# Kernel tuning notes

Hardware: AMD Instinct MI355X
Metric: run time of the kernel (lower is better)

Reference implementation:

```python
import jax, jax.numpy as jnp
import numpy as np

N_NODES = 20000
N_EDGES = 200000
N_GRAPHS = 128
IN_DIM = 256
HID = 512
HEADS = 8
C = HID // HEADS  # 64
LAT = 256
NEG_SLOPE = 0.2
BN_EPS = 1e-5


def setup_inputs() -> dict:
    key = jax.random.key(0)
    ks = jax.random.split(key, 24)
    n = lambda k, s, sc=0.05: jax.random.normal(k, s, jnp.float32) * sc
    return {
        'x': jax.random.normal(ks[0], (N_NODES, IN_DIM), jnp.float32),
        'edge_index': jax.random.randint(ks[1], (2, N_EDGES), 0, N_NODES, jnp.int32),
        'batch': jnp.sort(jax.random.randint(ks[2], (N_NODES,), 0, N_GRAPHS, jnp.int32)),
        'Wl0': n(ks[3], (IN_DIM, HID)), 'bl0': n(ks[4], (HID,)),
        'Wr0': n(ks[5], (IN_DIM, HID)), 'br0': n(ks[6], (HID,)),
        'att0': n(ks[7], (HEADS, C)), 'bias0': n(ks[8], (HID,)),
        'Wl1': n(ks[9], (HID, HID)), 'bl1': n(ks[10], (HID,)),
        'Wr1': n(ks[11], (HID, HID)), 'br1': n(ks[12], (HID,)),
        'att1': n(ks[13], (HEADS, C)), 'bias1': n(ks[14], (HID,)),
        'bn_gamma': jnp.ones((HID,), jnp.float32),
        'bn_beta': jnp.zeros((HID,), jnp.float32),
        'bn_mean': n(ks[15], (HID,)),
        'bn_var': jax.random.uniform(ks[16], (HID,), jnp.float32, 0.5, 1.5),
        'Wfc': n(ks[17], (HID, LAT)), 'bfc': n(ks[18], (LAT,)),
    }


def gatv2_layer(x, src, dst, Wl, bl, Wr, br, att, bias):
    # x: [N, F]; returns [N, HEADS*C]. GATv2: e = a . LeakyReLU(Wl x_src + Wr x_dst)
    xl = (x @ Wl + bl).reshape(-1, HEADS, C)  # source transform [N,H,C]
    xr = (x @ Wr + br).reshape(-1, HEADS, C)  # target transform [N,H,C]
    feat = jax.nn.leaky_relu(xl[src] + xr[dst], NEG_SLOPE)     # [E,H,C]
    logits = jnp.einsum('ehc,hc->eh', feat, att)               # [E,H]
    # segment softmax over incoming edges of each target node
    m = jax.ops.segment_max(logits, dst, num_segments=N_NODES)  # [N,H]
    p = jnp.exp(logits - m[dst])
    denom = jax.ops.segment_sum(p, dst, num_segments=N_NODES)   # [N,H]
    alpha = p / (denom[dst] + 1e-16)                            # [E,H]
    msg = xl[src] * alpha[:, :, None]                           # [E,H,C]
    out = jax.ops.segment_sum(msg, dst, num_segments=N_NODES)   # [N,H,C]
    return out.reshape(-1, HEADS * C) + bias


def reference(x, edge_index, batch, Wl0, bl0, Wr0, br0, att0, bias0,
              Wl1, bl1, Wr1, br1, att1, bias1,
              bn_gamma, bn_beta, bn_mean, bn_var, Wfc, bfc):
    src, dst = edge_index[0], edge_index[1]
    # layer 0 + ELU (dropout is identity in eval mode)
    h = jax.nn.elu(gatv2_layer(x, src, dst, Wl0, bl0, Wr0, br0, att0, bias0))
    # layer 1 + ELU
    h = jax.nn.elu(gatv2_layer(h, src, dst, Wl1, bl1, Wr1, br1, att1, bias1))
    # global add pool over graphs
    g = jax.ops.segment_sum(h, batch, num_segments=N_GRAPHS)  # [G, HID]
    # BatchNorm1d (eval mode: running stats)
    g = (g - bn_mean) * jax.lax.rsqrt(bn_var + BN_EPS) * bn_gamma + bn_beta
    return g @ Wfc + bfc  # [G, LAT]
```

## Files before the change

kernel.cpp:

```cpp
#include <hip/hip_runtime.h>
#include <hip/hip_bf16.h>
#include <cstdint>

#define NN 20000
#define NE 200000
#define NG 128
#define HID 512
#define XLR_W 1024

typedef __attribute__((ext_vector_type(4))) float f32x4;
typedef __attribute__((ext_vector_type(8))) short s16x8;

__device__ __forceinline__ float bf2f(unsigned short u) {
  union { unsigned int i; float f; } v; v.i = ((unsigned int)u) << 16; return v.f;
}
__device__ __forceinline__ unsigned short f2bf(float f) {
  union { float f; unsigned int i; } v; v.f = f;
  unsigned int i = v.i + 0x7FFFu + ((v.i >> 16) & 1u);
  return (unsigned short)(i >> 16);
}
__device__ __forceinline__ float asf(unsigned int u) {
  union { unsigned int i; float f; } v; v.i = u; return v.f;
}

__global__ void k_cast(const float* __restrict__ in, unsigned short* __restrict__ out, int n4) {
  int i = blockIdx.x * blockDim.x + threadIdx.x;
  if (i < n4) {
    float4 v = ((const float4*)in)[i];
    ushort4 o;
    o.x = f2bf(v.x); o.y = f2bf(v.y); o.z = f2bf(v.z); o.w = f2bf(v.w);
    ((ushort4*)out)[i] = o;
  }
}

__global__ void k_hist(const int* __restrict__ dst, int* __restrict__ deg, int E) {
  int i = blockIdx.x * blockDim.x + threadIdx.x;
  if (i < E) atomicAdd(&deg[dst[i]], 1);
}

__global__ void k_scan(const int* __restrict__ deg, int* __restrict__ offs,
                       int* __restrict__ woff, int n) {
  __shared__ int wsum[16];
  __shared__ int carry;
  int t = threadIdx.x;
  int wid = t >> 6, lane = t & 63;
  if (t == 0) carry = 0;
  __syncthreads();
  for (int base = 0; base < n; base += 1024) {
    int i = base + t;
    int v = (i < n) ? deg[i] : 0;
    int s = v;
#pragma unroll
    for (int off = 1; off < 64; off <<= 1) {
      int x = __shfl_up(s, off, 64);
      if (lane >= off) s += x;
    }
    if (lane == 63) wsum[wid] = s;
    __syncthreads();
    if (wid == 0) {
      int ws = (lane < 16) ? wsum[lane] : 0;
#pragma unroll
      for (int off = 1; off < 16; off <<= 1) {
        int x = __shfl_up(ws, off, 64);
        if (lane >= off) ws += x;
      }
      if (lane < 16) wsum[lane] = ws;
    }
    __syncthreads();
    int c0 = carry;
    int ex = s - v + (wid ? wsum[wid - 1] : 0) + c0;
    if (i < n) { offs[i] = ex; woff[i] = ex; }
    int tot = wsum[15];
    __syncthreads();
    if (t == 0) carry = c0 + tot;
    __syncthreads();
  }
  if (t == 0) offs[n] = carry;
}

__global__ void k_scatter(const int* __restrict__ src, const int* __restrict__ dst,
                          int* __restrict__ woff, int* __restrict__ src_s, int E) {
  int i = blockIdx.x * blockDim.x + threadIdx.x;
  if (i < E) {
    int d = dst[i];
    int pos = atomicAdd(&woff[d], 1);
    src_s[pos] = src[i];
  }
}

__global__ void k_pack(const float* __restrict__ Wl, const float* __restrict__ bl,
                       const float* __restrict__ Wr, const float* __restrict__ br,
                       unsigned short* __restrict__ wt, float* __restrict__ bcat, int kshift) {
  int id = blockIdx.x * blockDim.x + threadIdx.x;
  int K = 1 << kshift;
  int total = XLR_W << kshift;
  if (id < total) {
    int nrow = id >> kshift, k = id & (K - 1);
    float v = (nrow < HID) ? Wl[k * HID + nrow] : Wr[k * HID + (nrow - HID)];
    wt[id] = f2bf(v);
  }
  if (id < XLR_W) bcat[id] = (id < HID) ? bl[id] : br[id - HID];
}

#define BM 128
#define BN 128
#define BK 32
#define LSTR 40

__global__ __launch_bounds__(256, 2) void k_gemm(const unsigned short* __restrict__ A,
                                                 const unsigned short* __restrict__ Bt,
                                                 const float* __restrict__ bias,
                                                 unsigned short* __restrict__ C,
                                                 int M, int N, int K) {
  __shared__ __align__(16) unsigned short As[BM * LSTR];
  __shared__ __align__(16) unsigned short Bs[BN * LSTR];
  int m0 = blockIdx.y * BM, n0 = blockIdx.x * BN;
  int t = threadIdx.x;
  int wave = t >> 6, lane = t & 63;
  int wm = (wave >> 1) * 64, wn = (wave & 1) * 64;
  int ml = lane & 15, mq = lane >> 4;
  int srow = t >> 2;
  int scol = (t & 3) * 8;

  f32x4 acc[4][4];
#pragma unroll
  for (int i = 0; i < 4; i++)
#pragma unroll
    for (int j = 0; j < 4; j++) acc[i][j] = (f32x4)0.0f;

  int ar0 = m0 + srow; if (ar0 > M - 1) ar0 = M - 1;
  int ar1 = m0 + srow + 64; if (ar1 > M - 1) ar1 = M - 1;
  const int4* a0p = (const int4*)(A + (size_t)ar0 * K + scol);
  const int4* a1p = (const int4*)(A + (size_t)ar1 * K + scol);
  const int4* b0p = (const int4*)(Bt + (size_t)(n0 + srow) * K + scol);
  const int4* b1p = (const int4*)(Bt + (size_t)(n0 + srow + 64) * K + scol);

  for (int k0 = 0; k0 < K; k0 += BK) {
    int4 av0 = *a0p; int4 av1 = *a1p; int4 bv0 = *b0p; int4 bv1 = *b1p;
    a0p += BK / 8; a1p += BK / 8; b0p += BK / 8; b1p += BK / 8;
    *(int4*)(&As[srow * LSTR + scol]) = av0;
    *(int4*)(&As[(srow + 64) * LSTR + scol]) = av1;
    *(int4*)(&Bs[srow * LSTR + scol]) = bv0;
    *(int4*)(&Bs[(srow + 64) * LSTR + scol]) = bv1;
    __syncthreads();
    s16x8 af[4], bfr[4];
#pragma unroll
    for (int i = 0; i < 4; i++)
      af[i] = *(const s16x8*)(&As[(wm + i * 16 + ml) * LSTR + mq * 8]);
#pragma unroll
    for (int j = 0; j < 4; j++)
      bfr[j] = *(const s16x8*)(&Bs[(wn + j * 16 + ml) * LSTR + mq * 8]);
#pragma unroll
    for (int i = 0; i < 4; i++)
#pragma unroll
      for (int j = 0; j < 4; j++)
        acc[i][j] = __builtin_amdgcn_mfma_f32_16x16x32_bf16(af[i], bfr[j], acc[i][j], 0, 0, 0);
    __syncthreads();
  }

#pragma unroll
  for (int i = 0; i < 4; i++) {
#pragma unroll
    for (int j = 0; j < 4; j++) {
      int col = n0 + wn + j * 16 + ml;
      float bcol = bias[col];
#pragma unroll
      for (int r = 0; r < 4; r++) {
        int row = m0 + wm + i * 16 + mq * 4 + r;
        if (row < M) C[(size_t)row * N + col] = f2bf(acc[i][j][r] + bcol);
      }
    }
  }
}

__global__ __launch_bounds__(256) void k_attn(const unsigned short* __restrict__ xlr,
                                              const float* __restrict__ att,
                                              const int* __restrict__ offs,
                                              const int* __restrict__ src_s,
                                              const float* __restrict__ bias,
                                              unsigned short* __restrict__ hout) {
  __shared__ float red[4][8][68];
  __shared__ float reds[4][8];
  int n = blockIdx.x;
  int wave = threadIdx.x >> 6, lane = threadIdx.x & 63;
  int h = lane >> 3, k = lane & 7;
  int c = h * 64 + k * 8;
  int s0 = offs[n], s1 = offs[n + 1];

  uint4 uxr = *(const uint4*)(xlr + (size_t)n * XLR_W + HID + c);
  float xr[8];
  xr[0] = asf(uxr.x << 16); xr[1] = asf(uxr.x & 0xFFFF0000u);
  xr[2] = asf(uxr.y << 16); xr[3] = asf(uxr.y & 0xFFFF0000u);
  xr[4] = asf(uxr.z << 16); xr[5] = asf(uxr.z & 0xFFFF0000u);
  xr[6] = asf(uxr.w << 16); xr[7] = asf(uxr.w & 0xFFFF0000u);
  float at[8];
  {
    const float4* ap = (const float4*)(att + c);
    float4 a0 = ap[0], a1 = ap[1];
    at[0] = a0.x; at[1] = a0.y; at[2] = a0.z; at[3] = a0.w;
    at[4] = a1.x; at[5] = a1.y; at[6] = a1.z; at[7] = a1.w;
  }

  float acc[8] = {0.f, 0.f, 0.f, 0.f, 0.f, 0.f, 0.f, 0.f};
  float sum = 0.0f;

  int i = s0 + wave;
  uint4 u_cur = make_uint4(0, 0, 0, 0);
  if (i < s1) {
    int s = src_s[i];
    u_cur = *(const uint4*)(xlr + (size_t)s * XLR_W + c);
  }
  int nx = i + 4;
  for (; i < s1; i += 4) {
    uint4 u = u_cur;
    if (nx < s1) {
      int s = src_s[nx];
      u_cur = *(const uint4*)(xlr + (size_t)s * XLR_W + c);
    }
    nx += 4;

    float xl[8];
    xl[0] = asf(u.x << 16); xl[1] = asf(u.x & 0xFFFF0000u);
    xl[2] = asf(u.y << 16); xl[3] = asf(u.y & 0xFFFF0000u);
    xl[4] = asf(u.z << 16); xl[5] = asf(u.z & 0xFFFF0000u);
    xl[6] = asf(u.w << 16); xl[7] = asf(u.w & 0xFFFF0000u);

    float l = 0.0f;
#pragma unroll
    for (int j = 0; j < 8; j++) {
      float v = xl[j] + xr[j];
      v = fmaf(0.4f, fabsf(v), 0.6f * v);
      l = fmaf(v, at[j], l);
    }
    l += __shfl_xor(l, 1, 64);
    l += __shfl_xor(l, 2, 64);
    l += __shfl_xor(l, 4, 64);

    float p = __expf(l);
    sum += p;
#pragma unroll
    for (int j = 0; j < 8; j++) acc[j] = fmaf(p, xl[j], acc[j]);
  }

#pragma unroll
  for (int j = 0; j < 8; j++) red[wave][h][k * 8 + j] = acc[j];
  if (k == 0) reds[wave][h] = sum;
  __syncthreads();

  int t = threadIdx.x;
  int cc = t * 2;
  int hh = cc >> 6, off = cc & 63;
  float a0 = red[0][hh][off] + red[1][hh][off] + red[2][hh][off] + red[3][hh][off];
  float a1 = red[0][hh][off + 1] + red[1][hh][off + 1] + red[2][hh][off + 1] + red[3][hh][off + 1];
  float sm = reds[0][hh] + reds[1][hh] + reds[2][hh] + reds[3][hh];
  float di = 1.0f / (sm + 1e-16f);
  float o_a = a0 * di + bias[cc];
  float o_b = a1 * di + bias[cc + 1];
  o_a = o_a > 0.0f ? o_a : (__expf(o_a) - 1.0f);
  o_b = o_b > 0.0f ? o_b : (__expf(o_b) - 1.0f);
  unsigned int up = (unsigned int)f2bf(o_a) | ((unsigned int)f2bf(o_b) << 16);
  *(unsigned int*)(hout + (size_t)n * HID + cc) = up;
}

__device__ __forceinline__ int lower_bound(const int* __restrict__ a, int n, int key) {
  int lo = 0, hi = n;
  while (lo < hi) { int mid = (lo + hi) >> 1; if (a[mid] < key) lo = mid + 1; else hi = mid; }
  return lo;
}

__global__ __launch_bounds__(256) void k_pool(const unsigned short* __restrict__ h,
                                              const int* __restrict__ batch,
                                              float* __restrict__ part) {
  int g = blockIdx.x, p = blockIdx.y, t = threadIdx.x;
  int start = lower_bound(batch, NN, g);
  int end = lower_bound(batch, NN, g + 1);
  int mid = start + ((end - start + 1) >> 1);
  int lo = p ? mid : start;
  int hi = p ? end : mid;
  int c = t * 2;
  float a0 = 0.0f, a1 = 0.0f;
  for (int n = lo; n < hi; n++) {
    unsigned int u = *(const unsigned int*)(h + (size_t)n * HID + c);
    a0 += asf(u << 16);
    a1 += asf(u & 0xFFFF0000u);
  }
  float* dstp = part + ((size_t)g * 2 + p) * HID + c;
  dstp[0] = a0;
  dstp[1] = a1;
}

__global__ __launch_bounds__(256) void k_fc(const float* __restrict__ part,
                                            const float* __restrict__ gamma,
                                            const float* __restrict__ beta,
                                            const float* __restrict__ mean,
                                            const float* __restrict__ var,
                                            const float* __restrict__ Wfc,
                                            const float* __restrict__ bfc,
                                            float* __restrict__ out) {
  __shared__ float xsm[512];
  int g = blockIdx.x, t = threadIdx.x;
  for (int c = t; c < HID; c += 256) {
    float s = part[(size_t)g * 2 * HID + c] + part[((size_t)g * 2 + 1) * HID + c];
    xsm[c] = (s - mean[c]) * rsqrtf(var[c] + 1e-5f) * gamma[c] + beta[c];
  }
  __syncthreads();
  float acc = bfc[t];
#pragma unroll 8
  for (int k = 0; k < 512; k++) acc += xsm[k] * Wfc[k * 256 + t];
  out[g * 256 + t] = acc;
}

extern "C" void kernel_launch(void* const* d_in, const int* in_sizes, int n_in,
                              void* d_out, int out_size, void* d_ws, size_t ws_size,
                              hipStream_t stream) {
  const float* x     = (const float*)d_in[0];
  const int* ei      = (const int*)d_in[1];
  const int* batch   = (const int*)d_in[2];
  const float* Wl0   = (const float*)d_in[3];
  const float* bl0   = (const float*)d_in[4];
  const float* Wr0   = (const float*)d_in[5];
  const float* br0   = (const float*)d_in[6];
  const float* att0  = (const float*)d_in[7];
  const float* bias0 = (const float*)d_in[8];
  const float* Wl1   = (const float*)d_in[9];
  const float* bl1   = (const float*)d_in[10];
  const float* Wr1   = (const float*)d_in[11];
  const float* br1   = (const float*)d_in[12];
  const float* att1  = (const float*)d_in[13];
  const float* bias1 = (const float*)d_in[14];
  const float* gamma = (const float*)d_in[15];
  const float* beta  = (const float*)d_in[16];
  const float* mean  = (const float*)d_in[17];
  const float* var   = (const float*)d_in[18];
  const float* Wfc   = (const float*)d_in[19];
  const float* bfc   = (const float*)d_in[20];

  const int* src = ei;
  const int* dst = ei + NE;

  char* w = (char*)d_ws;
  size_t off = 0;
  auto alloc = [&](size_t bytes) -> void* {
    void* p = w + off;
    off += (bytes + 255) & ~(size_t)255;
    return p;
  };
  int* deg            = (int*)alloc((size_t)NN * 4);
  int* offs           = (int*)alloc((size_t)(NN + 1) * 4);
  int* woff           = (int*)alloc((size_t)NN * 4);
  int* src_s          = (int*)alloc((size_t)NE * 4);
  unsigned short* xb  = (unsigned short*)alloc((size_t)NN * 256 * 2);
  unsigned short* xlr = (unsigned short*)alloc((size_t)NN * XLR_W * 2);
  unsigned short* hb  = (unsigned short*)alloc((size_t)NN * HID * 2);
  unsigned short* wt  = (unsigned short*)alloc((size_t)XLR_W * HID * 2);
  float* bcat         = (float*)alloc((size_t)XLR_W * 4);
  float* part         = (float*)alloc((size_t)NG * 2 * HID * 4);

  hipMemsetAsync(deg, 0, (size_t)NN * 4, stream);
  k_hist<<<(NE + 255) / 256, 256, 0, stream>>>(dst, deg, NE);
  k_scan<<<1, 1024, 0, stream>>>(deg, offs, woff, NN);
  k_scatter<<<(NE + 255) / 256, 256, 0, stream>>>(src, dst, woff, src_s, NE);

  k_cast<<<(NN * 256 / 4 + 255) / 256, 256, 0, stream>>>(x, xb, NN * 256 / 4);

  k_pack<<<(XLR_W * 256 + 255) / 256, 256, 0, stream>>>(Wl0, bl0, Wr0, br0, wt, bcat, 8);
  k_gemm<<<dim3(XLR_W / BN, (NN + BM - 1) / BM), 256, 0, stream>>>(xb, wt, bcat, xlr, NN, XLR_W, 256);
  k_attn<<<NN, 256, 0, stream>>>(xlr, att0, offs, src_s, bias0, hb);

  k_pack<<<(XLR_W * 512 + 255) / 256, 256, 0, stream>>>(Wl1, bl1, Wr1, br1, wt, bcat, 9);
  k_gemm<<<dim3(XLR_W / BN, (NN + BM - 1) / BM), 256, 0, stream>>>(hb, wt, bcat, xlr, NN, XLR_W, 512);
  k_attn<<<NN, 256, 0, stream>>>(xlr, att1, offs, src_s, bias1, hb);

  k_pool<<<dim3(NG, 2), 256, 0, stream>>>(hb, batch, part);
  k_fc<<<NG, 256, 0, stream>>>(part, gamma, beta, mean, var, Wfc, bfc, (float*)d_out);
}
```

Baseline: 358.1 us.

## Parallelize CSR scan, use direct global-to-LDS loads in GEMM, widen pooling split

```diff
diff --git a/kernel.cpp b/kernel.cpp
--- a/kernel.cpp
+++ b/kernel.cpp
@@ -22,6 +22,11 @@
 __device__ __forceinline__ float asf(unsigned int u) {
   union { unsigned int i; float f; } v; v.i = u; return v.f;
 }
+
+#define GLOAD16(gp, lp)                                                        \
+  __builtin_amdgcn_global_load_lds(                                            \
+      (const __attribute__((address_space(1))) unsigned int*)(gp),             \
+      (__attribute__((address_space(3))) unsigned int*)(lp), 16, 0, 0)
 
 __global__ void k_cast(const float* __restrict__ in, unsigned short* __restrict__ out, int n4) {
   int i = blockIdx.x * blockDim.x + threadIdx.x;
@@ -38,44 +43,60 @@
   if (i < E) atomicAdd(&deg[dst[i]], 1);
 }
 
-__global__ void k_scan(const int* __restrict__ deg, int* __restrict__ offs,
-                       int* __restrict__ woff, int n) {
+__global__ __launch_bounds__(1024) void k_scan1(const int* __restrict__ deg,
+                                                int* __restrict__ offs,
+                                                int* __restrict__ btot, int n) {
   __shared__ int wsum[16];
-  __shared__ int carry;
   int t = threadIdx.x;
   int wid = t >> 6, lane = t & 63;
-  if (t == 0) carry = 0;
+  int i = blockIdx.x * 1024 + t;
+  int v = (i < n) ? deg[i] : 0;
+  int s = v;
+#pragma unroll
+  for (int off = 1; off < 64; off <<= 1) {
+    int x = __shfl_up(s, off, 64);
+    if (lane >= off) s += x;
+  }
+  if (lane == 63) wsum[wid] = s;
   __syncthreads();
-  for (int base = 0; base < n; base += 1024) {
-    int i = base + t;
-    int v = (i < n) ? deg[i] : 0;
-    int s = v;
-#pragma unroll
-    for (int off = 1; off < 64; off <<= 1) {
-      int x = __shfl_up(s, off, 64);
-      if (lane >= off) s += x;
+  if (wid == 0) {
+    int ws = (lane < 16) ? wsum[lane] : 0;
+#pragma unroll
+    for (int off = 1; off < 16; off <<= 1) {
+      int x = __shfl_up(ws, off, 64);
+      if (lane >= off) ws += x;
     }
-    if (lane == 63) wsum[wid] = s;
-    __syncthreads();
-    if (wid == 0) {
-      int ws = (lane < 16) ? wsum[lane] : 0;
-#pragma unroll
-      for (int off = 1; off < 16; off <<= 1) {
-        int x = __shfl_up(ws, off, 64);
-        if (lane >= off) ws += x;
-      }
-      if (lane < 16) wsum[lane] = ws;
-    }
-    __syncthreads();
-    int c0 = carry;
-    int ex = s - v + (wid ? wsum[wid - 1] : 0) + c0;
-    if (i < n) { offs[i] = ex; woff[i] = ex; }
-    int tot = wsum[15];
-    __syncthreads();
-    if (t == 0) carry = c0 + tot;
-    __syncthreads();
-  }
-  if (t == 0) offs[n] = carry;
+    if (lane < 16) wsum[lane] = ws;
+  }
+  __syncthreads();
+  int ex = s - v + (wid ? wsum[wid - 1] : 0);
+  if (i < n) offs[i] = ex;
+  if (t == 1023) btot[blockIdx.x] = ex + v;
+}
+
+__global__ void k_scan2(const int* __restrict__ btot, int* __restrict__ bofs,
+                        int nb, int* __restrict__ offs, int n) {
+  int lane = threadIdx.x;
+  int v = (lane < nb) ? btot[lane] : 0;
+  int s = v;
+#pragma unroll
+  for (int off = 1; off < 32; off <<= 1) {
+    int x = __shfl_up(s, off, 64);
+    if (lane >= off) s += x;
+  }
+  if (lane < nb) bofs[lane] = s - v;
+  if (lane == nb - 1) offs[n] = s;
+}
+
+__global__ __launch_bounds__(1024) void k_scan3(int* __restrict__ offs,
+                                                const int* __restrict__ bofs,
+                                                int* __restrict__ woff, int n) {
+  int i = blockIdx.x * 1024 + threadIdx.x;
+  if (i < n) {
+    int v = offs[i] + bofs[blockIdx.x];
+    offs[i] = v;
+    woff[i] = v;
+  }
 }
 
 __global__ void k_scatter(const int* __restrict__ src, const int* __restrict__ dst,
@@ -105,22 +126,21 @@
 #define BM 128
 #define BN 128
 #define BK 32
-#define LSTR 40
-
-__global__ __launch_bounds__(256, 2) void k_gemm(const unsigned short* __restrict__ A,
-                                                 const unsigned short* __restrict__ Bt,
-                                                 const float* __restrict__ bias,
-                                                 unsigned short* __restrict__ C,
-                                                 int M, int N, int K) {
-  __shared__ __align__(16) unsigned short As[BM * LSTR];
-  __shared__ __align__(16) unsigned short Bs[BN * LSTR];
+
+__global__ __launch_bounds__(256) void k_gemm(const unsigned short* __restrict__ A,
+                                              const unsigned short* __restrict__ Bt,
+                                              const float* __restrict__ bias,
+                                              unsigned short* __restrict__ C,
+                                              int M, int N, int K) {
+  __shared__ __align__(16) unsigned short As[BM * BK];
+  __shared__ __align__(16) unsigned short Bs[BN * BK];
   int m0 = blockIdx.y * BM, n0 = blockIdx.x * BN;
   int t = threadIdx.x;
   int wave = t >> 6, lane = t & 63;
   int wm = (wave >> 1) * 64, wn = (wave & 1) * 64;
   int ml = lane & 15, mq = lane >> 4;
-  int srow = t >> 2;
-  int scol = (t & 3) * 8;
+  int lr = lane >> 2;
+  int lc = (lane & 3) * 8;
 
   f32x4 acc[4][4];
 #pragma unroll
@@ -128,28 +148,31 @@
 #pragma unroll
     for (int j = 0; j < 4; j++) acc[i][j] = (f32x4)0.0f;
 
-  int ar0 = m0 + srow; if (ar0 > M - 1) ar0 = M - 1;
-  int ar1 = m0 + srow + 64; if (ar1 > M - 1) ar1 = M - 1;
-  const int4* a0p = (const int4*)(A + (size_t)ar0 * K + scol);
-  const int4* a1p = (const int4*)(A + (size_t)ar1 * K + scol);
-  const int4* b0p = (const int4*)(Bt + (size_t)(n0 + srow) * K + scol);
-  const int4* b1p = (const int4*)(Bt + (size_t)(n0 + srow + 64) * K + scol);
+  int ar0 = m0 + wave * 32 + lr;      if (ar0 > M - 1) ar0 = M - 1;
+  int ar1 = m0 + wave * 32 + 16 + lr; if (ar1 > M - 1) ar1 = M - 1;
+  const unsigned short* ga0 = A + (size_t)ar0 * K + lc;
+  const unsigned short* ga1 = A + (size_t)ar1 * K + lc;
+  const unsigned short* gb0 = Bt + (size_t)(n0 + wave * 32 + lr) * K + lc;
+  const unsigned short* gb1 = gb0 + (size_t)16 * K;
+  unsigned short* la0 = &As[(wave * 32) * BK];
+  unsigned short* la1 = &As[(wave * 32 + 16) * BK];
+  unsigned short* lb0 = &Bs[(wave * 32) * BK];
+  unsigned short* lb1 = &Bs[(wave * 32 + 16) * BK];
 
   for (int k0 = 0; k0 < K; k0 += BK) {
-    int4 av0 = *a0p; int4 av1 = *a1p; int4 bv0 = *b0p; int4 bv1 = *b1p;
-    a0p += BK / 8; a1p += BK / 8; b0p += BK / 8; b1p += BK / 8;
-    *(int4*)(&As[srow * LSTR + scol]) = av0;
-    *(int4*)(&As[(srow + 64) * LSTR + scol]) = av1;
-    *(int4*)(&Bs[srow * LSTR + scol]) = bv0;
-    *(int4*)(&Bs[(srow + 64) * LSTR + scol]) = bv1;
+    GLOAD16(ga0, la0);
+    GLOAD16(ga1, la1);
+    GLOAD16(gb0, lb0);
+    GLOAD16(gb1, lb1);
+    ga0 += BK; ga1 += BK; gb0 += BK; gb1 += BK;
     __syncthreads();
     s16x8 af[4], bfr[4];
 #pragma unroll
     for (int i = 0; i < 4; i++)
-      af[i] = *(const s16x8*)(&As[(wm + i * 16 + ml) * LSTR + mq * 8]);
+      af[i] = *(const s16x8*)(&As[(wm + i * 16 + ml) * BK + mq * 8]);
 #pragma unroll
     for (int j = 0; j < 4; j++)
-      bfr[j] = *(const s16x8*)(&Bs[(wn + j * 16 + ml) * LSTR + mq * 8]);
+      bfr[j] = *(const s16x8*)(&Bs[(wn + j * 16 + ml) * BK + mq * 8]);
 #pragma unroll
     for (int i = 0; i < 4; i++)
 #pragma unroll
@@ -274,9 +297,9 @@
   int g = blockIdx.x, p = blockIdx.y, t = threadIdx.x;
   int start = lower_bound(batch, NN, g);
   int end = lower_bound(batch, NN, g + 1);
-  int mid = start + ((end - start + 1) >> 1);
-  int lo = p ? mid : start;
-  int hi = p ? end : mid;
+  int cntq = (end - start + 3) >> 2;
+  int lo = start + p * cntq;
+  int hi = lo + cntq; if (hi > end) hi = end;
   int c = t * 2;
   float a0 = 0.0f, a1 = 0.0f;
   for (int n = lo; n < hi; n++) {
@@ -284,7 +307,7 @@
     a0 += asf(u << 16);
     a1 += asf(u & 0xFFFF0000u);
   }
-  float* dstp = part + ((size_t)g * 2 + p) * HID + c;
+  float* dstp = part + ((size_t)g * 4 + p) * HID + c;
   dstp[0] = a0;
   dstp[1] = a1;
 }
@@ -300,7 +323,8 @@
   __shared__ float xsm[512];
   int g = blockIdx.x, t = threadIdx.x;
   for (int c = t; c < HID; c += 256) {
-    float s = part[(size_t)g * 2 * HID + c] + part[((size_t)g * 2 + 1) * HID + c];
+    float s = part[((size_t)g * 4 + 0) * HID + c] + part[((size_t)g * 4 + 1) * HID + c]
+            + part[((size_t)g * 4 + 2) * HID + c] + part[((size_t)g * 4 + 3) * HID + c];
     xsm[c] = (s - mean[c]) * rsqrtf(var[c] + 1e-5f) * gamma[c] + beta[c];
   }
   __syncthreads();
@@ -349,16 +373,22 @@
   int* offs           = (int*)alloc((size_t)(NN + 1) * 4);
   int* woff           = (int*)alloc((size_t)NN * 4);
   int* src_s          = (int*)alloc((size_t)NE * 4);
+  int* btot           = (int*)alloc((size_t)32 * 4);
+  int* bofs           = (int*)alloc((size_t)32 * 4);
   unsigned short* xb  = (unsigned short*)alloc((size_t)NN * 256 * 2);
   unsigned short* xlr = (unsigned short*)alloc((size_t)NN * XLR_W * 2);
   unsigned short* hb  = (unsigned short*)alloc((size_t)NN * HID * 2);
   unsigned short* wt  = (unsigned short*)alloc((size_t)XLR_W * HID * 2);
   float* bcat         = (float*)alloc((size_t)XLR_W * 4);
-  float* part         = (float*)alloc((size_t)NG * 2 * HID * 4);
+  float* part         = (float*)alloc((size_t)NG * 4 * HID * 4);
+
+  const int NB = (NN + 1023) / 1024;
 
   hipMemsetAsync(deg, 0, (size_t)NN * 4, stream);
   k_hist<<<(NE + 255) / 256, 256, 0, stream>>>(dst, deg, NE);
-  k_scan<<<1, 1024, 0, stream>>>(deg, offs, woff, NN);
+  k_scan1<<<NB, 1024, 0, stream>>>(deg, offs, btot, NN);
+  k_scan2<<<1, 64, 0, stream>>>(btot, bofs, NB, offs, NN);
+  k_scan3<<<NB, 1024, 0, stream>>>(offs, bofs, woff, NN);
   k_scatter<<<(NE + 255) / 256, 256, 0, stream>>>(src, dst, woff, src_s, NE);
 
   k_cast<<<(NN * 256 / 4 + 255) / 256, 256, 0, stream>>>(x, xb, NN * 256 / 4);
@@ -371,6 +401,6 @@
   k_gemm<<<dim3(XLR_W / BN, (NN + BM - 1) / BM), 256, 0, stream>>>(hb, wt, bcat, xlr, NN, XLR_W, 512);
   k_attn<<<NN, 256, 0, stream>>>(xlr, att1, offs, src_s, bias1, hb);
 
-  k_pool<<<dim3(NG, 2), 256, 0, stream>>>(hb, batch, part);
+  k_pool<<<dim3(NG, 4), 256, 0, stream>>>(hb, batch, part);
   k_fc<<<NG, 256, 0, stream>>>(part, gamma, beta, mean, var, Wfc, bfc, (float*)d_out);
 }
```

Result: faster. 336.9 us (-5.9%).
